# Performance work log

Measured on AMD Instinct MI355X. Metric: run time of the kernel, lower is better.

## Reference

```python
import jax, jax.numpy as jnp
import numpy as np

D_MODEL = 2048
NHEAD = 32
N_KV = 8
HEAD_DIM = D_MODEL // NHEAD
EPS = 1e-5


def setup_inputs() -> dict:
    key = jax.random.key(0)
    k1, k2, k3, k4, k5 = jax.random.split(key, 5)
    B, S = 2, 2048
    return {
        "x": jax.random.normal(k1, (B, S, D_MODEL), dtype=jnp.float32),
        "wq": jax.random.normal(k2, (D_MODEL, D_MODEL), dtype=jnp.float32) * 0.02,
        "wk": jax.random.normal(k3, (N_KV * HEAD_DIM, D_MODEL), dtype=jnp.float32) * 0.02,
        "wv": jax.random.normal(k4, (N_KV * HEAD_DIM, D_MODEL), dtype=jnp.float32) * 0.02,
        "wo": jax.random.normal(k5, (D_MODEL, D_MODEL), dtype=jnp.float32) * 0.02,
    }


def weight_quant(w):
    # ternary/binary quant with straight-through estimator
    scale = jnp.maximum(jnp.mean(jnp.abs(w)), EPS)
    return jax.lax.stop_gradient(jnp.sign(w) * scale - w) + w


def bitlinear(x, w):
    # F.linear(x, weight_quant(w)) = x @ w_q.T
    return x @ weight_quant(w).T


def reference(x, wq, wk, wv, wo):
    B, S, _ = x.shape
    G = NHEAD // N_KV  # kv groups
    # projections
    q = bitlinear(x, wq).reshape(B, S, N_KV, G, HEAD_DIM)   # [B,S,Kv,G,D]
    k = bitlinear(x, wk).reshape(B, S, N_KV, HEAD_DIM)      # [B,S,Kv,D]
    v = bitlinear(x, wv).reshape(B, S, N_KV, HEAD_DIM)
    # GQA causal attention without materializing repeated K/V
    sm_scale = 1.0 / jnp.sqrt(jnp.asarray(HEAD_DIM, dtype=x.dtype))
    scores = jnp.einsum('bskgd,btkd->bkgst', q, k) * sm_scale  # [B,Kv,G,S,S]
    causal = jnp.tril(jnp.ones((S, S), dtype=bool))
    scores = jnp.where(causal, scores, jnp.asarray(-jnp.inf, dtype=scores.dtype))
    probs = jax.nn.softmax(scores, axis=-1)
    out = jnp.einsum('bkgst,btkd->bskgd', probs, v)  # [B,S,Kv,G,D]
    out = out.reshape(B, S, D_MODEL)
    return bitlinear(out, wo)
```

## Files before the change

kernel.cpp:

```cpp
#include <hip/hip_runtime.h>
#include <stdint.h>


#define D_MODEL 2048
#define S_LEN   2048
#define BATCH   2
#define NKV     8
#define HD      64
#define MROWS   (BATCH * S_LEN)
#define NQKV    3072
#define LDQKV   3072

typedef unsigned short u16;
typedef __bf16 bf16x8 __attribute__((ext_vector_type(8)));
typedef float  f32x4  __attribute__((ext_vector_type(4)));
typedef float  f32x16 __attribute__((ext_vector_type(16)));
typedef unsigned u32x4 __attribute__((ext_vector_type(4)));

__device__ __forceinline__ u16 f2bf(float f) {
  union { float f; unsigned u; } v; v.f = f;
  unsigned r = v.u + 0x7FFFu + ((v.u >> 16) & 1u);
  return (u16)(r >> 16);
}

__device__ __forceinline__ float exp2_fast(float x) {
  float r; asm("v_exp_f32 %0, %1" : "=v"(r) : "v"(x)); return r;
}

__device__ __forceinline__ unsigned cvt_pk_bf16(float a, float b) {
  unsigned r;
  asm("v_cvt_pk_bf16_f32 %0, %1, %2" : "=v"(r) : "v"(a), "v"(b));
  return r;
}

__device__ __forceinline__ void lds_load16(u16* lds, const u16* g) {
  __builtin_amdgcn_global_load_lds(
      (const __attribute__((address_space(1))) void*)g,
      (__attribute__((address_space(3))) void*)lds, 16, 0, 0);
}

#define SM_LOG2E 0.180336880f
#define THR_LOG2 11.5415603f

__global__ void prep_all(const float* __restrict__ wq, const float* __restrict__ wk,
                         const float* __restrict__ wv, const float* __restrict__ wo,
                         const float* __restrict__ x,
                         u16* __restrict__ wqkvs, u16* __restrict__ wos,
                         u16* __restrict__ xb, double* __restrict__ partials) {
  const int bid = blockIdx.x;
  const float* src; u16* dst; int n4, rb, nb; bool sgn = true;
  if (bid < 256)      { src = wq; dst = wqkvs;                  n4 = 1048576; rb = bid;       nb = 256; }
  else if (bid < 320) { src = wk; dst = wqkvs + 2048 * D_MODEL; n4 = 262144;  rb = bid - 256; nb = 64;  }
  else if (bid < 384) { src = wv; dst = wqkvs + 2560 * D_MODEL; n4 = 262144;  rb = bid - 320; nb = 64;  }
  else if (bid < 640) { src = wo; dst = wos;                    n4 = 1048576; rb = bid - 384; nb = 256; }
  else                { src = x;  dst = xb;                     n4 = 2097152; rb = bid - 640; nb = 512; sgn = false; }

  if (sgn) {
    double s = 0.0;
    for (int i = rb * 256 + threadIdx.x; i < n4; i += nb * 256) {
      float4 v = reinterpret_cast<const float4*>(src)[i];
      ushort4 o;
      o.x = v.x > 0.f ? 0x3F80 : (v.x < 0.f ? 0xBF80 : 0);
      o.y = v.y > 0.f ? 0x3F80 : (v.y < 0.f ? 0xBF80 : 0);
      o.z = v.z > 0.f ? 0x3F80 : (v.z < 0.f ? 0xBF80 : 0);
      o.w = v.w > 0.f ? 0x3F80 : (v.w < 0.f ? 0xBF80 : 0);
      reinterpret_cast<ushort4*>(dst)[i] = o;
      s += (double)fabsf(v.x) + (double)fabsf(v.y) +
           (double)fabsf(v.z) + (double)fabsf(v.w);
    }
    __shared__ double sm[256];
    sm[threadIdx.x] = s;
    __syncthreads();
    for (int off = 128; off > 0; off >>= 1) {
      if (threadIdx.x < off) sm[threadIdx.x] += sm[threadIdx.x + off];
      __syncthreads();
    }
    if (threadIdx.x == 0) partials[bid] = sm[0];
  } else {
    for (int i = rb * 256 + threadIdx.x; i < n4; i += nb * 256) {
      float4 v = reinterpret_cast<const float4*>(src)[i];
      ushort4 o;
      o.x = f2bf(v.x); o.y = f2bf(v.y); o.z = f2bf(v.z); o.w = f2bf(v.w);
      reinterpret_cast<ushort4*>(dst)[i] = o;
    }
  }
}

__global__ void finalize_scales(const double* __restrict__ partials,
                                float* __restrict__ tabs) {
  __shared__ float sc_sh[4];
  const int w = threadIdx.x >> 6;
  const int lane = threadIdx.x & 63;
  const int beg[4] = {0, 256, 320, 384};
  const int cnt[4] = {256, 64, 64, 256};
  const double counts[4] = {4194304.0, 1048576.0, 1048576.0, 4194304.0};
  double s = 0.0;
  for (int i = lane; i < cnt[w]; i += 64) s += partials[beg[w] + i];
  for (int off = 1; off < 64; off <<= 1) s += __shfl_xor(s, off);
  if (lane == 0) sc_sh[w] = fmaxf((float)(s / counts[w]), 1e-5f);
  __syncthreads();
  if (threadIdx.x == 0) {
    const float s0 = sc_sh[0], s1 = sc_sh[1], s2 = sc_sh[2], s3 = sc_sh[3];
    for (int i = 0; i < 24; ++i)
      tabs[i] = (i < 16) ? s0 * SM_LOG2E : (i < 20 ? s1 : s2);
    for (int i = 0; i < 16; ++i) tabs[24 + i] = s3;
  }
}

template <int OUT_BF16, int VSPLIT>
__global__ __launch_bounds__(256, 4) void gemm_bt(
    const u16* __restrict__ A, const u16* __restrict__ Bt, void* __restrict__ Cv,
    const float* __restrict__ tab, u16* __restrict__ vt, int M, int N, int K) {
  __shared__ u16 lA[128 * 64];
  __shared__ u16 lB[128 * 64];
  const int tid = threadIdx.x;
  const int lane = tid & 63, wave = tid >> 6;
  const int lo = lane & 15, hi = lane >> 4;
  const int m0 = blockIdx.y * 128, n0 = blockIdx.x * 128;
  const int wr = (wave >> 1) * 64, wc = (wave & 1) * 64;

  f32x4 acc[4][4] = {};

  for (int k0 = 0; k0 < K; k0 += 64) {
#pragma unroll
    for (int it = 0; it < 4; ++it) {
      const int c = it * 256 + wave * 64 + lane;
      const int row = c >> 3, kc = (c & 7) << 3;
      lds_load16(&lA[(it * 256 + wave * 64) * 8], &A[(size_t)(m0 + row) * K + k0 + kc]);
      lds_load16(&lB[(it * 256 + wave * 64) * 8], &Bt[(size_t)(n0 + row) * K + k0 + kc]);
    }
    __syncthreads();
#pragma unroll
    for (int kk = 0; kk < 2; ++kk) {
      bf16x8 af[4], bfr[4];
#pragma unroll
      for (int i = 0; i < 4; ++i)
        af[i] = *reinterpret_cast<const bf16x8*>(&lA[(wr + i * 16 + lo) * 64 + kk * 32 + hi * 8]);
#pragma unroll
      for (int i = 0; i < 4; ++i)
        bfr[i] = *reinterpret_cast<const bf16x8*>(&lB[(wc + i * 16 + lo) * 64 + kk * 32 + hi * 8]);
#pragma unroll
      for (int mi = 0; mi < 4; ++mi)
#pragma unroll
        for (int ni = 0; ni < 4; ++ni)
          acc[mi][ni] = __builtin_amdgcn_mfma_f32_16x16x32_bf16(af[mi], bfr[ni], acc[mi][ni], 0, 0, 0);
    }
    __syncthreads();
  }

  const float scale = tab[blockIdx.x];
  if (VSPLIT && (int)blockIdx.x >= 20) {
#pragma unroll
    for (int mi = 0; mi < 4; ++mi) {
#pragma unroll
      for (int ni = 0; ni < 4; ++ni) {
        const int col = (n0 - 2560) + wc + ni * 16 + lo;
        const int row = m0 + wr + mi * 16 + hi * 4;
        unsigned w01 = (unsigned)f2bf(acc[mi][ni][0] * scale) |
                       ((unsigned)f2bf(acc[mi][ni][1] * scale) << 16);
        unsigned w23 = (unsigned)f2bf(acc[mi][ni][2] * scale) |
                       ((unsigned)f2bf(acc[mi][ni][3] * scale) << 16);
        uint2 pk; pk.x = w01; pk.y = w23;
        *reinterpret_cast<uint2*>(vt + (size_t)col * MROWS + row) = pk;
      }
    }
    return;
  }
#pragma unroll
  for (int mi = 0; mi < 4; ++mi) {
#pragma unroll
    for (int ni = 0; ni < 4; ++ni) {
#pragma unroll
      for (int r = 0; r < 4; ++r) {
        const int row = m0 + wr + mi * 16 + hi * 4 + r;
        const int col = n0 + wc + ni * 16 + lo;
        const float v = acc[mi][ni][r] * scale;
        if (OUT_BF16)
          reinterpret_cast<u16*>(Cv)[(size_t)row * N + col] = f2bf(v);
        else
          reinterpret_cast<float*>(Cv)[(size_t)row * N + col] = v;
      }
    }
  }
}

__device__ __forceinline__ void stage_tile(u16* dst, const u16* base, int ld,
                                           int tid, int wave) {
#pragma unroll
  for (int it = 0; it < 2; ++it) {
    const int c = it * 256 + tid;
    const int row = c >> 3;
    const int ch = (c & 7) ^ (row & 7);
    lds_load16(dst + (it * 256 + wave * 64) * 8, base + (size_t)row * ld + ch * 8);
  }
}

#define TILE_BODY(MASKED)                                                      \
  {                                                                            \
    const int t0 = ti * 64;                                                    \
    const int cur = ti & 1;                                                    \
    u16* lKc = (u16*)lK[cur];                                                  \
    u16* lVc = (u16*)lV[cur];                                                  \
    f32x16 sacc[2] = {};                                                       \
    __builtin_amdgcn_s_setprio(1);                                             \
    _Pragma("unroll")                                                          \
    for (int w = 0; w < 4; ++w) {                                              \
      _Pragma("unroll")                                                        \
      for (int nf = 0; nf < 2; ++nf) {                                         \
        bf16x8 kf = *reinterpret_cast<const bf16x8*>(                          \
            &lKc[(nf * 32 + q31) * 64 + ((w * 16 + hi5 * 8) ^ swl)]);          \
        sacc[nf] = __builtin_amdgcn_mfma_f32_32x32x16_bf16(                    \
            kf, qf[w], sacc[nf], 0, 0, 0);                                     \
      }                                                                        \
    }                                                                          \
    __builtin_amdgcn_s_setprio(0);                                             \
    if (ti + 1 < nt) {                                                         \
      stage_tile(lK[cur ^ 1], Kb + (size_t)(brow + t0 + 64) * LDQKV, LDQKV,    \
                 tid, wave);                                                   \
      stage_tile(lV[cur ^ 1], Vb + t0 + 64, MROWS, tid, wave);                 \
    }                                                                          \
    if (MASKED) {                                                              \
      _Pragma("unroll")                                                        \
      for (int nf = 0; nf < 2; ++nf) {                                         \
        _Pragma("unroll")                                                      \
        for (int rg = 0; rg < 16; ++rg) {                                      \
          const int tg = t0 + nf * 32 + (rg >> 2) * 8 + hi5 * 4 + (rg & 3);    \
          if (tg > qg) sacc[nf][rg] = -1e30f;                                  \
        }                                                                      \
      }                                                                        \
    }                                                                          \
    float mt = -1e30f;                                                         \
    _Pragma("unroll")                                                          \
    for (int nf = 0; nf < 2; ++nf) {                                           \
      _Pragma("unroll")                                                        \
      for (int rg = 0; rg < 16; ++rg) mt = fmaxf(mt, sacc[nf][rg]);            \
    }                                                                          \
    mt = fmaxf(mt, __shfl_xor(mt, 32));                                        \
    if (!__all((int)(mt <= m_run + THR_LOG2))) {                               \
      const float mn = fmaxf(m_run, mt);                                       \
      const float alpha = exp2_fast(m_run - mn);                               \
      m_run = mn;                                                              \
      l_lane *= alpha;                                                         \
      _Pragma("unroll")                                                        \
      for (int nf = 0; nf < 2; ++nf) {                                         \
        _Pragma("unroll")                                                      \
        for (int rg = 0; rg < 16; ++rg) oacc[nf][rg] *= alpha;                 \
      }                                                                        \
    }                                                                          \
    unsigned pk[2][8];                                                         \
    _Pragma("unroll")                                                          \
    for (int nf = 0; nf < 2; ++nf) {                                           \
      _Pragma("unroll")                                                        \
      for (int c = 0; c < 4; ++c) {                                            \
        const float e0 = exp2_fast(sacc[nf][4 * c + 0] - m_run);               \
        const float e1 = exp2_fast(sacc[nf][4 * c + 1] - m_run);               \
        const float e2 = exp2_fast(sacc[nf][4 * c + 2] - m_run);               \
        const float e3 = exp2_fast(sacc[nf][4 * c + 3] - m_run);               \
        l_lane += (e0 + e1) + (e2 + e3);                                       \
        pk[nf][2 * c + 0] = cvt_pk_bf16(e0, e1);                               \
        pk[nf][2 * c + 1] = cvt_pk_bf16(e2, e3);                               \
      }                                                                        \
    }                                                                          \
    __builtin_amdgcn_s_setprio(1);                                             \
    _Pragma("unroll")                                                          \
    for (int w = 0; w < 4; ++w) {                                              \
      const int nf = w >> 1, c4 = (w & 1) * 4;                                 \
      unsigned a0 = pk[nf][c4 + 0], a1 = pk[nf][c4 + 1];                       \
      unsigned b0 = pk[nf][c4 + 2], b1 = pk[nf][c4 + 3];                       \
      asm volatile("v_permlane32_swap_b32 %0, %1" : "+v"(a0), "+v"(b0));       \
      asm volatile("v_permlane32_swap_b32 %0, %1" : "+v"(a1), "+v"(b1));       \
      u32x4 pw; pw.x = a0; pw.y = a1; pw.z = b0; pw.w = b1;                    \
      bf16x8 pfr = *reinterpret_cast<const bf16x8*>(&pw);                      \
      _Pragma("unroll")                                                        \
      for (int nfo = 0; nfo < 2; ++nfo) {                                      \
        bf16x8 vf = *reinterpret_cast<const bf16x8*>(                          \
            &lVc[(nfo * 32 + q31) * 64 + ((w * 16 + hi5 * 8) ^ swl)]);         \
        oacc[nfo] = __builtin_amdgcn_mfma_f32_32x32x16_bf16(                   \
            vf, pfr, oacc[nfo], 0, 0, 0);                                      \
      }                                                                        \
    }                                                                          \
    __builtin_amdgcn_s_setprio(0);                                             \
    __syncthreads();                                                           \
  }

__global__ __launch_bounds__(256, 2) void flash_attn(
    const u16* __restrict__ QKV, const u16* __restrict__ VT,
    u16* __restrict__ Og) {
  __shared__ u16 lK[2][64 * 64];
  __shared__ u16 lV[2][64 * 64];

  const int tid = threadIdx.x;
  const int lane = tid & 63, wave = tid >> 6;
  const int q31 = lane & 31, hi5 = lane >> 5;
  const int lin = (int)blockIdx.y * 8 + (int)blockIdx.x;
  const int xcd = lin & 7, slot = lin >> 3;
  const int G = xcd * 2 + (slot >> 5);
  const int wb = slot & 31;
  const int b = G >> 3, kv = G & 7;
  const int h = kv * 4 + (wb >> 3);
  const int lbx = wb & 7;
  const int brow = b * S_LEN;
  const u16* Q  = QKV + h * HD;
  const u16* Kb = QKV + 2048 + kv * HD;
  const u16* Vb = VT + (size_t)(kv * HD) * MROWS + brow;
  const int swl = (lane & 7) << 3;

#pragma unroll 1
  for (int pi = 0; pi < 2; ++pi) {
    const int qt = pi == 0 ? lbx : (15 - lbx);
    const int q0 = qt * 128;
    const int q0w = q0 + wave * 32;
    const int nt = 2 * qt + 2;
    const int qg = q0w + q31;

    bf16x8 qf[4];
    {
      const size_t qr = (size_t)(brow + q0w + q31) * LDQKV;
#pragma unroll
      for (int w = 0; w < 4; ++w)
        qf[w] = *reinterpret_cast<const bf16x8*>(&Q[qr + w * 16 + hi5 * 8]);
    }

    f32x16 oacc[2] = {};
    float m_run = -1e30f, l_lane = 0.f;

    stage_tile(lK[0], Kb + (size_t)brow * LDQKV, LDQKV, tid, wave);
    stage_tile(lV[0], Vb, MROWS, tid, wave);
    __syncthreads();

#pragma unroll 1
    for (int ti = 0; ti < 2 * qt; ++ti) TILE_BODY(0)
#pragma unroll 1
    for (int ti = 2 * qt; ti < nt; ++ti) TILE_BODY(1)

    {
      float ls = l_lane;
      ls += __shfl_xor(ls, 32);
      const float inv = 1.f / ls;
#pragma unroll
      for (int nfo = 0; nfo < 2; ++nfo) {
#pragma unroll
        for (int c = 0; c < 4; ++c) {
          const unsigned u0 = cvt_pk_bf16(oacc[nfo][4 * c + 0] * inv,
                                          oacc[nfo][4 * c + 1] * inv);
          const unsigned u1 = cvt_pk_bf16(oacc[nfo][4 * c + 2] * inv,
                                          oacc[nfo][4 * c + 3] * inv);
          const int d = nfo * 32 + c * 8 + hi5 * 4;
          uint2 st; st.x = u0; st.y = u1;
          *reinterpret_cast<uint2*>(
              &Og[(size_t)(brow + q0w + q31) * D_MODEL + h * HD + d]) = st;
        }
      }
    }
  }
}

extern "C" void kernel_launch(void* const* d_in, const int* in_sizes, int n_in,
                              void* d_out, int out_size, void* d_ws, size_t ws_size,
                              hipStream_t stream) {
  (void)in_sizes; (void)n_in; (void)out_size; (void)ws_size;
  const float* x  = (const float*)d_in[0];
  const float* wq = (const float*)d_in[1];
  const float* wk = (const float*)d_in[2];
  const float* wv = (const float*)d_in[3];
  const float* wo = (const float*)d_in[4];
  float* out = (float*)d_out;
  char* ws = (char*)d_ws;

  double* partials = (double*)ws;
  float* tabs = (float*)(ws + 6144);
  size_t off = 8192;
  u16* xb    = (u16*)(ws + off); off += (size_t)MROWS * D_MODEL * 2;
  u16* wqkvs = (u16*)(ws + off); off += (size_t)NQKV * D_MODEL * 2;
  u16* wos   = (u16*)(ws + off); off += (size_t)D_MODEL * D_MODEL * 2;
  u16* qkvb  = (u16*)(ws + off); off += (size_t)MROWS * NQKV * 2;
  u16* ao    = (u16*)(ws + off); off += (size_t)MROWS * D_MODEL * 2;
  u16* vt    = (u16*)(ws + off); off += (size_t)512 * MROWS * 2;

  prep_all<<<1152, 256, 0, stream>>>(wq, wk, wv, wo, x, wqkvs, wos, xb, partials);
  finalize_scales<<<1, 256, 0, stream>>>(partials, tabs);

  gemm_bt<1, 1><<<dim3(NQKV / 128, MROWS / 128), 256, 0, stream>>>(
      xb, wqkvs, qkvb, tabs, vt, MROWS, NQKV, D_MODEL);

  flash_attn<<<dim3(8, 64), 256, 0, stream>>>(qkvb, vt, ao);

  gemm_bt<0, 0><<<dim3(D_MODEL / 128, MROWS / 128), 256, 0, stream>>>(
      ao, wos, out, tabs + 24, nullptr, MROWS, D_MODEL, D_MODEL);
}
```

Measured before the change: 185.3 us.

## Double-buffer GEMM LDS tiles with 512-thread blocks and XOR swizzle

The shared GEMM kernel becomes an 8-wave, 512-thread block with two LDS buffers, so the async global-to-LDS load of the tile two steps ahead runs while the current tile is computed. Waits use an explicit vmcnt count and raw s_barrier in place of full syncthreads. The LDS layout gets an XOR swizzle to cut bank conflicts on fragment reads, and setprio is raised around the MFMA block. In exchange LDS use doubles to 64KB per block, which may lower occupancy, and the hand-written vmcnt count has to match the number of outstanding loads exactly.

```diff
diff --git a/kernel.cpp b/kernel.cpp
--- a/kernel.cpp
+++ b/kernel.cpp
@@ -108,52 +108,89 @@
 }
 
 template <int OUT_BF16, int VSPLIT>
-__global__ __launch_bounds__(256, 4) void gemm_bt(
+__global__ __launch_bounds__(512, 4) void gemm_dp(
     const u16* __restrict__ A, const u16* __restrict__ Bt, void* __restrict__ Cv,
     const float* __restrict__ tab, u16* __restrict__ vt, int M, int N, int K) {
-  __shared__ u16 lA[128 * 64];
-  __shared__ u16 lB[128 * 64];
+  __shared__ u16 lA[2][128 * 64];
+  __shared__ u16 lB[2][128 * 64];
   const int tid = threadIdx.x;
   const int lane = tid & 63, wave = tid >> 6;
   const int lo = lane & 15, hi = lane >> 4;
   const int m0 = blockIdx.y * 128, n0 = blockIdx.x * 128;
-  const int wr = (wave >> 1) * 64, wc = (wave & 1) * 64;
-
-  f32x4 acc[4][4] = {};
-
-  for (int k0 = 0; k0 < K; k0 += 64) {
-#pragma unroll
-    for (int it = 0; it < 4; ++it) {
-      const int c = it * 256 + wave * 64 + lane;
-      const int row = c >> 3, kc = (c & 7) << 3;
-      lds_load16(&lA[(it * 256 + wave * 64) * 8], &A[(size_t)(m0 + row) * K + k0 + kc]);
-      lds_load16(&lB[(it * 256 + wave * 64) * 8], &Bt[(size_t)(n0 + row) * K + k0 + kc]);
-    }
-    __syncthreads();
+  const int wr = (wave >> 2) * 64;
+  const int wc = (wave & 3) * 32;
+  const int swl = (lo & 7) << 3;
+
+  f32x4 acc[4][2] = {};
+  const int nt = K >> 6;
+
+#define STAGE(bf, kt)                                                          \
+  {                                                                            \
+    const int k0s = (kt) * 64;                                                 \
+    _Pragma("unroll")                                                          \
+    for (int it = 0; it < 2; ++it) {                                           \
+      const int c = it * 512 + tid;                                            \
+      const int row = c >> 3;                                                  \
+      const int ch = (c & 7) ^ (row & 7);                                      \
+      lds_load16(&lA[bf][(it * 512 + wave * 64) * 8],                          \
+                 &A[(size_t)(m0 + row) * K + k0s + ch * 8]);                   \
+    }                                                                          \
+    _Pragma("unroll")                                                          \
+    for (int it = 0; it < 2; ++it) {                                           \
+      const int c = it * 512 + tid;                                            \
+      const int row = c >> 3;                                                  \
+      const int ch = (c & 7) ^ (row & 7);                                      \
+      lds_load16(&lB[bf][(it * 512 + wave * 64) * 8],                          \
+                 &Bt[(size_t)(n0 + row) * K + k0s + ch * 8]);                  \
+    }                                                                          \
+  }
+
+  STAGE(0, 0)
+  STAGE(1, 1)
+
+#pragma unroll 1
+  for (int kt = 0; kt < nt; ++kt) {
+    const int cur = kt & 1;
+    if (kt + 1 < nt)
+      asm volatile("s_waitcnt vmcnt(4)\n\ts_barrier" ::: "memory");
+    else
+      asm volatile("s_waitcnt vmcnt(0)\n\ts_barrier" ::: "memory");
+    __builtin_amdgcn_sched_barrier(0);
+
+    const u16* la = lA[cur];
+    const u16* lb = lB[cur];
 #pragma unroll
     for (int kk = 0; kk < 2; ++kk) {
-      bf16x8 af[4], bfr[4];
+      bf16x8 af[4], bfr[2];
 #pragma unroll
       for (int i = 0; i < 4; ++i)
-        af[i] = *reinterpret_cast<const bf16x8*>(&lA[(wr + i * 16 + lo) * 64 + kk * 32 + hi * 8]);
-#pragma unroll
-      for (int i = 0; i < 4; ++i)
-        bfr[i] = *reinterpret_cast<const bf16x8*>(&lB[(wc + i * 16 + lo) * 64 + kk * 32 + hi * 8]);
+        af[i] = *reinterpret_cast<const bf16x8*>(
+            &la[(wr + i * 16 + lo) * 64 + ((kk * 32 + hi * 8) ^ swl)]);
+#pragma unroll
+      for (int i = 0; i < 2; ++i)
+        bfr[i] = *reinterpret_cast<const bf16x8*>(
+            &lb[(wc + i * 16 + lo) * 64 + ((kk * 32 + hi * 8) ^ swl)]);
+      __builtin_amdgcn_s_setprio(1);
 #pragma unroll
       for (int mi = 0; mi < 4; ++mi)
 #pragma unroll
-        for (int ni = 0; ni < 4; ++ni)
-          acc[mi][ni] = __builtin_amdgcn_mfma_f32_16x16x32_bf16(af[mi], bfr[ni], acc[mi][ni], 0, 0, 0);
-    }
-    __syncthreads();
-  }
+        for (int ni = 0; ni < 2; ++ni)
+          acc[mi][ni] = __builtin_amdgcn_mfma_f32_16x16x32_bf16(
+              af[mi], bfr[ni], acc[mi][ni], 0, 0, 0);
+      __builtin_amdgcn_s_setprio(0);
+    }
+    __builtin_amdgcn_sched_barrier(0);
+    asm volatile("s_barrier" ::: "memory");
+    if (kt + 2 < nt) STAGE(cur, kt + 2)
+  }
+#undef STAGE
 
   const float scale = tab[blockIdx.x];
   if (VSPLIT && (int)blockIdx.x >= 20) {
 #pragma unroll
     for (int mi = 0; mi < 4; ++mi) {
 #pragma unroll
-      for (int ni = 0; ni < 4; ++ni) {
+      for (int ni = 0; ni < 2; ++ni) {
         const int col = (n0 - 2560) + wc + ni * 16 + lo;
         const int row = m0 + wr + mi * 16 + hi * 4;
         unsigned w01 = (unsigned)f2bf(acc[mi][ni][0] * scale) |
@@ -169,7 +206,7 @@
 #pragma unroll
   for (int mi = 0; mi < 4; ++mi) {
 #pragma unroll
-    for (int ni = 0; ni < 4; ++ni) {
+    for (int ni = 0; ni < 2; ++ni) {
 #pragma unroll
       for (int r = 0; r < 4; ++r) {
         const int row = m0 + wr + mi * 16 + hi * 4 + r;
@@ -380,11 +417,11 @@
   prep_all<<<1152, 256, 0, stream>>>(wq, wk, wv, wo, x, wqkvs, wos, xb, partials);
   finalize_scales<<<1, 256, 0, stream>>>(partials, tabs);
 
-  gemm_bt<1, 1><<<dim3(NQKV / 128, MROWS / 128), 256, 0, stream>>>(
+  gemm_dp<1, 1><<<dim3(NQKV / 128, MROWS / 128), 512, 0, stream>>>(
       xb, wqkvs, qkvb, tabs, vt, MROWS, NQKV, D_MODEL);
 
   flash_attn<<<dim3(8, 64), 256, 0, stream>>>(qkvb, vt, ao);
 
-  gemm_bt<0, 0><<<dim3(D_MODEL / 128, MROWS / 128), 256, 0, stream>>>(
+  gemm_dp<0, 0><<<dim3(D_MODEL / 128, MROWS / 128), 512, 0, stream>>>(
       ao, wos, out, tabs + 24, nullptr, MROWS, D_MODEL, D_MODEL);
 }
```

Result: faster. 175.7 us (-5.2%).
